# Kernel optimization log

Measured on AMD Instinct MI355X. Metric: run time of the kernel, lower is better.

Reference implementation:

```python
import jax, jax.numpy as jnp
import numpy as np

SIGMA = 0.05  # gaussian bandwidth from the source


def _sqdist(a, b):
    # a: [B,N,D], b: [B,M,D] -> [B,N,M] squared euclidean distance
    a2 = jnp.sum(a * a, axis=-1)[:, :, None]
    b2 = jnp.sum(b * b, axis=-1)[:, None, :]
    return a2 + b2 - 2.0 * jnp.einsum('bnd,bmd->bnm', a, b)


def setup_inputs() -> dict:
    key = jax.random.key(0)
    k1, k2, k3, k4 = jax.random.split(key, 4)
    B, N, D = 2, 4096, 32
    points = jax.random.normal(k1, (B, N, 3), dtype=jnp.float32)
    pointfea1 = jax.random.normal(k2, (B, N, D), dtype=jnp.float32)
    pointfea2 = jax.random.normal(k3, (B, N, D), dtype=jnp.float32)
    weights = jax.random.uniform(k4, (B, N), dtype=jnp.float32) / N  # point-cloud mass weights
    return {"points": points, "pointfea1": pointfea1, "pointfea2": pointfea2, "weights": weights}


def reference(points, pointfea1, pointfea2, weights):
    # naive_corres: per-point spatial log-gaussian softmax vs feature log-softmax,
    # weighted squared difference, reduced over both pair axes -> [B]
    x = points / SIGMA
    point_loggauss = jax.nn.log_softmax(-_sqdist(x, x), axis=2)          # [B,N,N]
    fea_logsoftmax = jax.nn.log_softmax(-_sqdist(pointfea1, pointfea2), axis=2)  # [B,N,N]
    diff2 = (jnp.exp(point_loggauss) - jnp.exp(fea_logsoftmax)) ** 2
    l2_loss = jnp.sum(diff2 * weights[:, :, None], axis=2)  # sum over j
    return jnp.sum(l2_loss, axis=1)                          # sum over i -> [B]
```

## Files before the change

kernel.cpp:

```cpp
#include <hip/hip_runtime.h>

#define D    32
#define BLK  256
#define NCH  8
#define STJ  64
#define LOG2E 1.44269504088896340736f

typedef short short8  __attribute__((ext_vector_type(8)));
typedef float floatx4 __attribute__((ext_vector_type(4)));
typedef float v2f     __attribute__((ext_vector_type(2)));

__device__ __forceinline__ short f2bf(float v) {
    union { float f; unsigned u; } x; x.f = v;
    unsigned r = x.u + 0x7fffu + ((x.u >> 16) & 1u);
    return (short)(r >> 16);
}
__device__ __forceinline__ float bf2f(short h) {
    union { float f; unsigned u; } x;
    x.u = ((unsigned)(unsigned short)h) << 16;
    return x.f;
}
__device__ __forceinline__ float fast_exp2(float x) {
#if __has_builtin(__builtin_amdgcn_exp2f)
    return __builtin_amdgcn_exp2f(x);
#else
    return exp2f(x);
#endif
}

__global__ __launch_bounds__(BLK) void precompute_kernel(
    const float* __restrict__ points,
    const float* __restrict__ fea1,
    const float* __restrict__ fea2,
    short* __restrict__ sAj, short* __restrict__ sBi,
    short* __restrict__ fAh, short* __restrict__ fAl,
    short* __restrict__ fBh, short* __restrict__ fBl,
    float* __restrict__ fn2, float* __restrict__ nf1,
    float* __restrict__ acc, float* __restrict__ out,
    int BN, int Bsz)
{
    int r = blockIdx.x * BLK + threadIdx.x;
    if (r < Bsz) out[r] = 0.0f;
    if (r >= BN) return;
#pragma unroll
    for (int s = 0; s < 5; ++s) acc[s * BN + r] = 0.0f;

    const float s2l = sqrtf(2.0f * LOG2E);
    const int t = r >> 4, m = r & 15;
    const size_t fb = ((size_t)t * 64 + m) * 8;

    float x0 = points[3*r+0] * 20.f;
    float x1 = points[3*r+1] * 20.f;
    float x2 = points[3*r+2] * 20.f;
    float xn = (x0*x0 + x1*x1 + x2*x2) * LOG2E;
    float xs[3] = {x0*s2l, x1*s2l, x2*s2l};
    short h[3], l[3], ll[3];
#pragma unroll
    for (int c = 0; c < 3; ++c) {
        h[c] = f2bf(xs[c]);
        float rm = xs[c] - bf2f(h[c]);
        l[c] = f2bf(rm);
        rm -= bf2f(l[c]);
        ll[c] = f2bf(rm);
    }
    short xnh = f2bf(xn);
    float rn = xn - bf2f(xnh);
    short xnm = f2bf(rn);
    rn -= bf2f(xnm);
    short xnl = f2bf(rn);
    const short N1 = (short)0xBF80;

    short8 aq[4], bq[4];
    aq[0] = (short8){h[0],h[1],h[2], l[0],l[1],l[2], ll[0],ll[1]};
    aq[1] = (short8){ll[2], h[0],h[1],h[2], l[0],l[1],l[2], ll[0]};
    aq[2] = (short8){ll[1],ll[2], h[0],h[1],h[2], l[0],l[1],l[2]};
    aq[3] = (short8){ll[0],ll[1],ll[2], xnh,xnm,xnl, N1,N1};
    bq[0] = (short8){h[0],h[1],h[2], h[0],h[1],h[2], h[0],h[1]};
    bq[1] = (short8){h[2], l[0],l[1],l[2], l[0],l[1],l[2], l[0]};
    bq[2] = (short8){l[1],l[2], ll[0],ll[1],ll[2], ll[0],ll[1],ll[2]};
    bq[3] = (short8){ll[0],ll[1],ll[2], N1,N1,N1, xnh,xnm};
#pragma unroll
    for (int q = 0; q < 4; ++q) {
        *(short8*)&sAj[fb + q*128] = aq[q];
        *(short8*)&sBi[fb + q*128] = bq[q];
    }

    const float* p1 = fea1 + (size_t)r * D;
    const float* p2 = fea2 + (size_t)r * D;
    float n1 = 0.f, n2 = 0.f;
#pragma unroll
    for (int q = 0; q < 4; ++q) {
        float4 a0 = *(const float4*)(p1 + q*8);
        float4 a1 = *(const float4*)(p1 + q*8 + 4);
        float e1[8] = {a0.x,a0.y,a0.z,a0.w,a1.x,a1.y,a1.z,a1.w};
        short8 hh1, ll1;
#pragma unroll
        for (int k = 0; k < 8; ++k) {
            n1 = fmaf(e1[k], e1[k], n1);
            float v = e1[k] * s2l;
            short hv = f2bf(v);
            hh1[k] = hv;
            ll1[k] = f2bf(v - bf2f(hv));
        }
        *(short8*)&fBh[fb + q*128] = hh1;
        *(short8*)&fBl[fb + q*128] = ll1;

        float4 b0 = *(const float4*)(p2 + q*8);
        float4 b1 = *(const float4*)(p2 + q*8 + 4);
        float e2[8] = {b0.x,b0.y,b0.z,b0.w,b1.x,b1.y,b1.z,b1.w};
        short8 hh2, ll2;
#pragma unroll
        for (int k = 0; k < 8; ++k) {
            n2 = fmaf(e2[k], e2[k], n2);
            float v = e2[k] * s2l;
            short hv = f2bf(v);
            hh2[k] = hv;
            ll2[k] = f2bf(v - bf2f(hv));
        }
        *(short8*)&fAh[fb + q*128] = hh2;
        *(short8*)&fAl[fb + q*128] = ll2;
    }
    nf1[r] = n1 * LOG2E;
    fn2[r] = n2 * LOG2E;
}

__global__ __launch_bounds__(BLK) void pair_kernel(
    const short* __restrict__ sAj,
    const short* __restrict__ fAh,
    const short* __restrict__ fAl,
    const short* __restrict__ sBi,
    const short* __restrict__ fBh,
    const short* __restrict__ fBl,
    const float* __restrict__ fn2,
    const float* __restrict__ nf1,
    float* __restrict__ acc,
    int N, int BN)
{
    __shared__ __align__(16) short lAs[STJ * D];
    __shared__ __align__(16) short lAh[STJ * D];
    __shared__ __align__(16) short lAl[STJ * D];
    __shared__ float lFn[STJ];

    const int tid  = threadIdx.x;
    const int lane = tid & 63;
    const int wv   = tid >> 6;
    const int m    = lane & 15;
    const int q    = lane >> 4;

    const int ibpb  = N >> 6;
    const int b     = blockIdx.x / ibpb;
    const int itile = blockIdx.x * 4 + wv;
    const int JCH   = N / NCH;
    const int jc0   = blockIdx.y * JCH;

    const size_t ti = ((size_t)itile * 64 + lane) * 8;
    short8 Bs  = *(const short8*)&sBi[ti];
    short8 Bfh = *(const short8*)&fBh[ti];
    short8 Bfl = *(const short8*)&fBl[ti];
    float nfin = -nf1[itile * 16 + m];

    v2f  sAB = {0.f, 0.f};
    v2f  s2  = {0.f, 0.f};
    float sab = 0.f;

    const int tjbase = (b * N + jc0) >> 4;
    const short* gAs = sAj + (size_t)tjbase * 512;
    const short* gAh = fAh + (size_t)tjbase * 512;
    const short* gAl = fAl + (size_t)tjbase * 512;
    const float* gFn = fn2 + (size_t)b * N + jc0;

    for (int s0 = 0; s0 < JCH; s0 += STJ) {
        const int to = s0 * 4;
        ((uint4*)lAs)[tid] = ((const uint4*)gAs)[to + tid];
        ((uint4*)lAh)[tid] = ((const uint4*)gAh)[to + tid];
        ((uint4*)lAl)[tid] = ((const uint4*)gAl)[to + tid];
        if (tid < STJ) lFn[tid] = gFn[s0 + tid];
        __syncthreads();

#pragma unroll 2
        for (int tt = 0; tt < STJ/16; ++tt) {
            const short8 As = *(const short8*)&lAs[(tt*64 + lane)*8];
            const short8 Ah = *(const short8*)&lAh[(tt*64 + lane)*8];
            const short8 Al = *(const short8*)&lAl[(tt*64 + lane)*8];
            floatx4 fnq = *(const floatx4*)&lFn[tt*16 + q*4];

            floatx4 cs = {0.f, 0.f, 0.f, 0.f};
            cs = __builtin_amdgcn_mfma_f32_16x16x32_bf16(As, Bs, cs, 0, 0, 0);

            floatx4 cf = {nfin - fnq[0], nfin - fnq[1],
                          nfin - fnq[2], nfin - fnq[3]};
            cf = __builtin_amdgcn_mfma_f32_16x16x32_bf16(Ah, Bfh, cf, 0, 0, 0);
            cf = __builtin_amdgcn_mfma_f32_16x16x32_bf16(Ah, Bfl, cf, 0, 0, 0);
            cf = __builtin_amdgcn_mfma_f32_16x16x32_bf16(Al, Bfh, cf, 0, 0, 0);

#pragma unroll
            for (int r = 0; r < 4; ++r) {
                float ea = fast_exp2(cs[r]);
                float eb = fast_exp2(cf[r]);
                v2f e = {ea, eb};
                sAB += e;
                s2   = __builtin_elementwise_fma(e, e, s2);
                sab  = fmaf(ea, eb, sab);
            }
        }
        __syncthreads();
    }

    float vA = sAB.x, vB = sAB.y, v2a = s2.x, v2b = s2.y, vab = sab;
    vA  += __shfl_xor(vA, 16);  vA  += __shfl_xor(vA, 32);
    vB  += __shfl_xor(vB, 16);  vB  += __shfl_xor(vB, 32);
    v2a += __shfl_xor(v2a, 16); v2a += __shfl_xor(v2a, 32);
    v2b += __shfl_xor(v2b, 16); v2b += __shfl_xor(v2b, 32);
    vab += __shfl_xor(vab, 16); vab += __shfl_xor(vab, 32);
    if (lane < 16) {
        int row = itile * 16 + lane;
        atomicAdd(&acc[0*BN + row], vA);
        atomicAdd(&acc[1*BN + row], v2a);
        atomicAdd(&acc[2*BN + row], vB);
        atomicAdd(&acc[3*BN + row], v2b);
        atomicAdd(&acc[4*BN + row], vab);
    }
}

__global__ __launch_bounds__(BLK) void finalize_kernel(
    const float* __restrict__ acc,
    const float* __restrict__ weights,
    float* __restrict__ out,
    int N, int BN)
{
    int row = blockIdx.x * BLK + threadIdx.x;
    int b   = (blockIdx.x * BLK) / N;

    float A   = acc[0*BN + row];
    float S2a = acc[1*BN + row];
    float Bt  = acc[2*BN + row];
    float S2b = acc[3*BN + row];
    float Sab = acc[4*BN + row];
    float invA = 1.0f / A;
    float invB = 1.0f / Bt;
    float val  = S2a*invA*invA - 2.0f*Sab*invA*invB + S2b*invB*invB;
    float sum  = weights[row] * val;

    __shared__ float red[BLK/64];
    for (int off = 32; off > 0; off >>= 1)
        sum += __shfl_down(sum, off);
    if ((threadIdx.x & 63) == 0) red[threadIdx.x >> 6] = sum;
    __syncthreads();
    if (threadIdx.x == 0) {
        float s = 0.f;
#pragma unroll
        for (int w = 0; w < BLK/64; ++w) s += red[w];
        atomicAdd(&out[b], s);
    }
}

extern "C" void kernel_launch(void* const* d_in, const int* in_sizes, int n_in,
                              void* d_out, int out_size, void* d_ws, size_t ws_size,
                              hipStream_t stream) {
    const float* points  = (const float*)d_in[0];
    const float* fea1    = (const float*)d_in[1];
    const float* fea2    = (const float*)d_in[2];
    const float* weights = (const float*)d_in[3];
    float* out = (float*)d_out;

    int B  = out_size;
    int BN = in_sizes[3];
    int N  = BN / B;

    float* acc = (float*)d_ws;
    char*  p   = (char*)d_ws + (size_t)5 * BN * 4;
    short* sAj = (short*)p; p += (size_t)BN * 64;
    short* sBi = (short*)p; p += (size_t)BN * 64;
    short* fAh = (short*)p; p += (size_t)BN * 64;
    short* fAl = (short*)p; p += (size_t)BN * 64;
    short* fBh = (short*)p; p += (size_t)BN * 64;
    short* fBl = (short*)p; p += (size_t)BN * 64;
    float* fn2 = (float*)p; p += (size_t)BN * 4;
    float* nf1 = (float*)p;

    precompute_kernel<<<dim3((BN + BLK - 1) / BLK), dim3(BLK), 0, stream>>>(
        points, fea1, fea2, sAj, sBi, fAh, fAl, fBh, fBl, fn2, nf1,
        acc, out, BN, B);

    dim3 grid(BN / 64, NCH);
    pair_kernel<<<grid, dim3(BLK), 0, stream>>>(
        sAj, fAh, fAl, sBi, fBh, fBl, fn2, nf1, acc, N, BN);

    finalize_kernel<<<dim3(BN / BLK), dim3(BLK), 0, stream>>>(acc, weights, out, N, BN);
}
```

Baseline: 86.74 us.

## Swap pair-kernel tiling to share j tiles across waves, prefetch, split precompute

In the pair kernel each wave now keeps four i-tiles in registers and takes its own 16-column j tile from each staged LDS chunk. Before, each wave had one i-tile and looped over all four j tiles. The next global j chunk is prefetched into registers while the current one is computed, the j range is split over twice as many chunks, and the precompute kernel uses four threads per point with shuffle-reduced norms. The goal is more independent MFMA/exp work per wave, overlapped global loads and more parallelism, at the cost of more registers and twice as many atomics.

```diff
diff --git a/kernel.cpp b/kernel.cpp
--- a/kernel.cpp
+++ b/kernel.cpp
@@ -2,7 +2,7 @@
 
 #define D    32
 #define BLK  256
-#define NCH  8
+#define NCH  16
 #define STJ  64
 #define LOG2E 1.44269504088896340736f
 
@@ -39,15 +39,16 @@
     float* __restrict__ acc, float* __restrict__ out,
     int BN, int Bsz)
 {
-    int r = blockIdx.x * BLK + threadIdx.x;
-    if (r < Bsz) out[r] = 0.0f;
+    const int g = blockIdx.x * BLK + threadIdx.x;
+    const int r = g >> 2, q = g & 3;
     if (r >= BN) return;
-#pragma unroll
-    for (int s = 0; s < 5; ++s) acc[s * BN + r] = 0.0f;
+    if (g < Bsz) out[g] = 0.0f;
+    acc[q * BN + r] = 0.0f;
+    if (q == 0) acc[4 * BN + r] = 0.0f;
 
     const float s2l = sqrtf(2.0f * LOG2E);
     const int t = r >> 4, m = r & 15;
-    const size_t fb = ((size_t)t * 64 + m) * 8;
+    const size_t fb = ((size_t)t * 64 + m + 16*q) * 8;
 
     float x0 = points[3*r+0] * 20.f;
     float x1 = points[3*r+1] * 20.f;
@@ -70,58 +71,61 @@
     short xnl = f2bf(rn);
     const short N1 = (short)0xBF80;
 
-    short8 aq[4], bq[4];
-    aq[0] = (short8){h[0],h[1],h[2], l[0],l[1],l[2], ll[0],ll[1]};
-    aq[1] = (short8){ll[2], h[0],h[1],h[2], l[0],l[1],l[2], ll[0]};
-    aq[2] = (short8){ll[1],ll[2], h[0],h[1],h[2], l[0],l[1],l[2]};
-    aq[3] = (short8){ll[0],ll[1],ll[2], xnh,xnm,xnl, N1,N1};
-    bq[0] = (short8){h[0],h[1],h[2], h[0],h[1],h[2], h[0],h[1]};
-    bq[1] = (short8){h[2], l[0],l[1],l[2], l[0],l[1],l[2], l[0]};
-    bq[2] = (short8){l[1],l[2], ll[0],ll[1],ll[2], ll[0],ll[1],ll[2]};
-    bq[3] = (short8){ll[0],ll[1],ll[2], N1,N1,N1, xnh,xnm};
-#pragma unroll
-    for (int q = 0; q < 4; ++q) {
-        *(short8*)&sAj[fb + q*128] = aq[q];
-        *(short8*)&sBi[fb + q*128] = bq[q];
-    }
-
-    const float* p1 = fea1 + (size_t)r * D;
-    const float* p2 = fea2 + (size_t)r * D;
+    short8 aq, bq;
+    if (q == 0) {
+        aq = (short8){h[0],h[1],h[2], l[0],l[1],l[2], ll[0],ll[1]};
+        bq = (short8){h[0],h[1],h[2], h[0],h[1],h[2], h[0],h[1]};
+    } else if (q == 1) {
+        aq = (short8){ll[2], h[0],h[1],h[2], l[0],l[1],l[2], ll[0]};
+        bq = (short8){h[2], l[0],l[1],l[2], l[0],l[1],l[2], l[0]};
+    } else if (q == 2) {
+        aq = (short8){ll[1],ll[2], h[0],h[1],h[2], l[0],l[1],l[2]};
+        bq = (short8){l[1],l[2], ll[0],ll[1],ll[2], ll[0],ll[1],ll[2]};
+    } else {
+        aq = (short8){ll[0],ll[1],ll[2], xnh,xnm,xnl, N1,N1};
+        bq = (short8){ll[0],ll[1],ll[2], N1,N1,N1, xnh,xnm};
+    }
+    *(short8*)&sAj[fb] = aq;
+    *(short8*)&sBi[fb] = bq;
+
+    const float* p1 = fea1 + (size_t)r * D + q*8;
+    const float* p2 = fea2 + (size_t)r * D + q*8;
+    float4 a0 = *(const float4*)(p1);
+    float4 a1 = *(const float4*)(p1 + 4);
+    float e1[8] = {a0.x,a0.y,a0.z,a0.w,a1.x,a1.y,a1.z,a1.w};
     float n1 = 0.f, n2 = 0.f;
-#pragma unroll
-    for (int q = 0; q < 4; ++q) {
-        float4 a0 = *(const float4*)(p1 + q*8);
-        float4 a1 = *(const float4*)(p1 + q*8 + 4);
-        float e1[8] = {a0.x,a0.y,a0.z,a0.w,a1.x,a1.y,a1.z,a1.w};
-        short8 hh1, ll1;
-#pragma unroll
-        for (int k = 0; k < 8; ++k) {
-            n1 = fmaf(e1[k], e1[k], n1);
-            float v = e1[k] * s2l;
-            short hv = f2bf(v);
-            hh1[k] = hv;
-            ll1[k] = f2bf(v - bf2f(hv));
-        }
-        *(short8*)&fBh[fb + q*128] = hh1;
-        *(short8*)&fBl[fb + q*128] = ll1;
-
-        float4 b0 = *(const float4*)(p2 + q*8);
-        float4 b1 = *(const float4*)(p2 + q*8 + 4);
-        float e2[8] = {b0.x,b0.y,b0.z,b0.w,b1.x,b1.y,b1.z,b1.w};
-        short8 hh2, ll2;
-#pragma unroll
-        for (int k = 0; k < 8; ++k) {
-            n2 = fmaf(e2[k], e2[k], n2);
-            float v = e2[k] * s2l;
-            short hv = f2bf(v);
-            hh2[k] = hv;
-            ll2[k] = f2bf(v - bf2f(hv));
-        }
-        *(short8*)&fAh[fb + q*128] = hh2;
-        *(short8*)&fAl[fb + q*128] = ll2;
-    }
-    nf1[r] = n1 * LOG2E;
-    fn2[r] = n2 * LOG2E;
+    short8 hh, llv;
+#pragma unroll
+    for (int k = 0; k < 8; ++k) {
+        n1 = fmaf(e1[k], e1[k], n1);
+        float v = e1[k] * s2l;
+        short hv = f2bf(v);
+        hh[k] = hv;
+        llv[k] = f2bf(v - bf2f(hv));
+    }
+    *(short8*)&fBh[fb] = hh;
+    *(short8*)&fBl[fb] = llv;
+
+    float4 b0 = *(const float4*)(p2);
+    float4 b1 = *(const float4*)(p2 + 4);
+    float e2[8] = {b0.x,b0.y,b0.z,b0.w,b1.x,b1.y,b1.z,b1.w};
+#pragma unroll
+    for (int k = 0; k < 8; ++k) {
+        n2 = fmaf(e2[k], e2[k], n2);
+        float v = e2[k] * s2l;
+        short hv = f2bf(v);
+        hh[k] = hv;
+        llv[k] = f2bf(v - bf2f(hv));
+    }
+    *(short8*)&fAh[fb] = hh;
+    *(short8*)&fAl[fb] = llv;
+
+    n1 += __shfl_xor(n1, 1); n1 += __shfl_xor(n1, 2);
+    n2 += __shfl_xor(n2, 1); n2 += __shfl_xor(n2, 2);
+    if (q == 0) {
+        nf1[r] = n1 * LOG2E;
+        fn2[r] = n2 * LOG2E;
+    }
 }
 
 __global__ __launch_bounds__(BLK) void pair_kernel(
@@ -139,7 +143,7 @@
     __shared__ __align__(16) short lAs[STJ * D];
     __shared__ __align__(16) short lAh[STJ * D];
     __shared__ __align__(16) short lAl[STJ * D];
-    __shared__ float lFn[STJ];
+    __shared__ __align__(16) float lFn[STJ];
 
     const int tid  = threadIdx.x;
     const int lane = tid & 63;
@@ -147,78 +151,96 @@
     const int m    = lane & 15;
     const int q    = lane >> 4;
 
-    const int ibpb  = N >> 6;
-    const int b     = blockIdx.x / ibpb;
-    const int itile = blockIdx.x * 4 + wv;
-    const int JCH   = N / NCH;
-    const int jc0   = blockIdx.y * JCH;
-
-    const size_t ti = ((size_t)itile * 64 + lane) * 8;
-    short8 Bs  = *(const short8*)&sBi[ti];
-    short8 Bfh = *(const short8*)&fBh[ti];
-    short8 Bfl = *(const short8*)&fBl[ti];
-    float nfin = -nf1[itile * 16 + m];
-
-    v2f  sAB = {0.f, 0.f};
-    v2f  s2  = {0.f, 0.f};
-    float sab = 0.f;
+    const int ibpb   = N >> 6;
+    const int b      = blockIdx.x / ibpb;
+    const int itile0 = blockIdx.x * 4;
+    const int JCH    = N / NCH;
+    const int jc0    = blockIdx.y * JCH;
+
+    short8 Bs[4], Bfh[4], Bfl[4];
+    float nfin[4];
+#pragma unroll
+    for (int it = 0; it < 4; ++it) {
+        const size_t ti = ((size_t)(itile0 + it) * 64 + lane) * 8;
+        Bs[it]  = *(const short8*)&sBi[ti];
+        Bfh[it] = *(const short8*)&fBh[ti];
+        Bfl[it] = *(const short8*)&fBl[ti];
+        nfin[it] = -nf1[(itile0 + it) * 16 + m];
+    }
+
+    v2f  sAB[4] = {{0.f,0.f},{0.f,0.f},{0.f,0.f},{0.f,0.f}};
+    v2f  s2 [4] = {{0.f,0.f},{0.f,0.f},{0.f,0.f},{0.f,0.f}};
+    float sab[4] = {0.f,0.f,0.f,0.f};
 
     const int tjbase = (b * N + jc0) >> 4;
-    const short* gAs = sAj + (size_t)tjbase * 512;
-    const short* gAh = fAh + (size_t)tjbase * 512;
-    const short* gAl = fAl + (size_t)tjbase * 512;
+    const uint4* gAs = (const uint4*)(sAj + (size_t)tjbase * 512);
+    const uint4* gAh = (const uint4*)(fAh + (size_t)tjbase * 512);
+    const uint4* gAl = (const uint4*)(fAl + (size_t)tjbase * 512);
     const float* gFn = fn2 + (size_t)b * N + jc0;
 
+    uint4 pA = gAs[tid], pH = gAh[tid], pL = gAl[tid];
+    float pF = (tid < STJ) ? gFn[tid] : 0.f;
+
     for (int s0 = 0; s0 < JCH; s0 += STJ) {
-        const int to = s0 * 4;
-        ((uint4*)lAs)[tid] = ((const uint4*)gAs)[to + tid];
-        ((uint4*)lAh)[tid] = ((const uint4*)gAh)[to + tid];
-        ((uint4*)lAl)[tid] = ((const uint4*)gAl)[to + tid];
-        if (tid < STJ) lFn[tid] = gFn[s0 + tid];
+        ((uint4*)lAs)[tid] = pA;
+        ((uint4*)lAh)[tid] = pH;
+        ((uint4*)lAl)[tid] = pL;
+        if (tid < STJ) lFn[tid] = pF;
         __syncthreads();
 
-#pragma unroll 2
-        for (int tt = 0; tt < STJ/16; ++tt) {
-            const short8 As = *(const short8*)&lAs[(tt*64 + lane)*8];
-            const short8 Ah = *(const short8*)&lAh[(tt*64 + lane)*8];
-            const short8 Al = *(const short8*)&lAl[(tt*64 + lane)*8];
-            floatx4 fnq = *(const floatx4*)&lFn[tt*16 + q*4];
-
+        const int sn = s0 + STJ;
+        if (sn < JCH) {
+            const int to = sn * 4;
+            pA = gAs[to + tid]; pH = gAh[to + tid]; pL = gAl[to + tid];
+            pF = (tid < STJ) ? gFn[sn + tid] : 0.f;
+        }
+
+        const short8 As = *(const short8*)&lAs[(wv*64 + lane)*8];
+        const short8 Ah = *(const short8*)&lAh[(wv*64 + lane)*8];
+        const short8 Al = *(const short8*)&lAl[(wv*64 + lane)*8];
+        const floatx4 fnq = *(const floatx4*)&lFn[wv*16 + q*4];
+
+#pragma unroll
+        for (int it = 0; it < 4; ++it) {
             floatx4 cs = {0.f, 0.f, 0.f, 0.f};
-            cs = __builtin_amdgcn_mfma_f32_16x16x32_bf16(As, Bs, cs, 0, 0, 0);
-
-            floatx4 cf = {nfin - fnq[0], nfin - fnq[1],
-                          nfin - fnq[2], nfin - fnq[3]};
-            cf = __builtin_amdgcn_mfma_f32_16x16x32_bf16(Ah, Bfh, cf, 0, 0, 0);
-            cf = __builtin_amdgcn_mfma_f32_16x16x32_bf16(Ah, Bfl, cf, 0, 0, 0);
-            cf = __builtin_amdgcn_mfma_f32_16x16x32_bf16(Al, Bfh, cf, 0, 0, 0);
+            cs = __builtin_amdgcn_mfma_f32_16x16x32_bf16(As, Bs[it], cs, 0, 0, 0);
+
+            floatx4 cf = {nfin[it] - fnq[0], nfin[it] - fnq[1],
+                          nfin[it] - fnq[2], nfin[it] - fnq[3]};
+            cf = __builtin_amdgcn_mfma_f32_16x16x32_bf16(Ah, Bfh[it], cf, 0, 0, 0);
+            cf = __builtin_amdgcn_mfma_f32_16x16x32_bf16(Ah, Bfl[it], cf, 0, 0, 0);
+            cf = __builtin_amdgcn_mfma_f32_16x16x32_bf16(Al, Bfh[it], cf, 0, 0, 0);
 
 #pragma unroll
             for (int r = 0; r < 4; ++r) {
                 float ea = fast_exp2(cs[r]);
                 float eb = fast_exp2(cf[r]);
                 v2f e = {ea, eb};
-                sAB += e;
-                s2   = __builtin_elementwise_fma(e, e, s2);
-                sab  = fmaf(ea, eb, sab);
+                sAB[it] += e;
+                s2[it]   = __builtin_elementwise_fma(e, e, s2[it]);
+                sab[it]  = fmaf(ea, eb, sab[it]);
             }
         }
         __syncthreads();
     }
 
-    float vA = sAB.x, vB = sAB.y, v2a = s2.x, v2b = s2.y, vab = sab;
-    vA  += __shfl_xor(vA, 16);  vA  += __shfl_xor(vA, 32);
-    vB  += __shfl_xor(vB, 16);  vB  += __shfl_xor(vB, 32);
-    v2a += __shfl_xor(v2a, 16); v2a += __shfl_xor(v2a, 32);
-    v2b += __shfl_xor(v2b, 16); v2b += __shfl_xor(v2b, 32);
-    vab += __shfl_xor(vab, 16); vab += __shfl_xor(vab, 32);
-    if (lane < 16) {
-        int row = itile * 16 + lane;
-        atomicAdd(&acc[0*BN + row], vA);
-        atomicAdd(&acc[1*BN + row], v2a);
-        atomicAdd(&acc[2*BN + row], vB);
-        atomicAdd(&acc[3*BN + row], v2b);
-        atomicAdd(&acc[4*BN + row], vab);
+#pragma unroll
+    for (int it = 0; it < 4; ++it) {
+        float vA = sAB[it].x, vB = sAB[it].y;
+        float v2a = s2[it].x, v2b = s2[it].y, vab = sab[it];
+        vA  += __shfl_xor(vA, 16);  vA  += __shfl_xor(vA, 32);
+        vB  += __shfl_xor(vB, 16);  vB  += __shfl_xor(vB, 32);
+        v2a += __shfl_xor(v2a, 16); v2a += __shfl_xor(v2a, 32);
+        v2b += __shfl_xor(v2b, 16); v2b += __shfl_xor(v2b, 32);
+        vab += __shfl_xor(vab, 16); vab += __shfl_xor(vab, 32);
+        if (lane < 16) {
+            int row = (itile0 + it) * 16 + lane;
+            atomicAdd(&acc[0*BN + row], vA);
+            atomicAdd(&acc[1*BN + row], v2a);
+            atomicAdd(&acc[2*BN + row], vB);
+            atomicAdd(&acc[3*BN + row], v2b);
+            atomicAdd(&acc[4*BN + row], vab);
+        }
     }
 }
 
@@ -278,7 +300,7 @@
     float* fn2 = (float*)p; p += (size_t)BN * 4;
     float* nf1 = (float*)p;
 
-    precompute_kernel<<<dim3((BN + BLK - 1) / BLK), dim3(BLK), 0, stream>>>(
+    precompute_kernel<<<dim3((BN * 4 + BLK - 1) / BLK), dim3(BLK), 0, stream>>>(
         points, fea1, fea2, sAj, sBi, fAh, fAl, fBh, fBl, fn2, nf1,
         acc, out, BN, B);
 
```

Result: slower. 88.55 us (+2.1%).
